# Kernel optimization log

Measured on AMD Instinct MI355X. Metric: run time of the kernel, lower is better.

## Reference

```python
import jax, jax.numpy as jnp
import numpy as np

N = 50000      # nodes
E = 800000     # edges (before self-loops)
H = 4          # heads
C = 64         # hidden_unit per head
IN = 256       # input_dim
OUT = 64       # output_dim
NEG = 0.2      # LeakyReLU slope in GATConv
EPS = 1e-5     # BatchNorm eps


def setup_inputs() -> dict:
    key = jax.random.key(0)
    ks = jax.random.split(key, 12)
    s = 0.05
    HC = H * C
    return {
        'x': jax.random.normal(ks[0], (N, IN), dtype=jnp.float32),
        'edge_index': jax.random.randint(ks[1], (2, E), 0, N, dtype=jnp.int64),
        # GATConv layer 1
        'W1': jax.random.normal(ks[2], (IN, HC), dtype=jnp.float32) * s,
        'att_src1': jax.random.normal(ks[3], (H, C), dtype=jnp.float32) * s,
        'att_dst1': jax.random.normal(ks[4], (H, C), dtype=jnp.float32) * s,
        'b1': jnp.zeros((HC,), jnp.float32),
        # GATConv layer 2
        'W2': jax.random.normal(ks[5], (HC, HC), dtype=jnp.float32) * s,
        'att_src2': jax.random.normal(ks[6], (H, C), dtype=jnp.float32) * s,
        'att_dst2': jax.random.normal(ks[7], (H, C), dtype=jnp.float32) * s,
        'b2': jnp.zeros((HC,), jnp.float32),
        # BatchNorms
        'g1': jnp.ones((HC,), jnp.float32), 'beta1': jnp.zeros((HC,), jnp.float32),
        'g2': jnp.ones((HC,), jnp.float32), 'beta2': jnp.zeros((HC,), jnp.float32),
        # final Linear
        'Wl': jax.random.normal(ks[8], (HC, OUT), dtype=jnp.float32) * s,
        'bl': jnp.zeros((OUT,), jnp.float32),
    }


def gat_layer(x, src, dst, W, a_src, a_dst, b):
    # x: [N, F_in] -> per-head features [N, H, C]
    xh = (x @ W).reshape(-1, H, C)
    alpha_src = jnp.einsum('nhc,hc->nh', xh, a_src)   # [N, H]
    alpha_dst = jnp.einsum('nhc,hc->nh', xh, a_dst)   # [N, H]
    e = jax.nn.leaky_relu(alpha_src[src] + alpha_dst[dst], NEG)  # [Etot, H]
    # segment softmax over edges grouped by destination node
    m = jax.ops.segment_max(e, dst, num_segments=N)              # [N, H]
    ex = jnp.exp(e - m[dst])
    den = jax.ops.segment_sum(ex, dst, num_segments=N)           # [N, H]
    alpha = ex / (den[dst] + 1e-16)                              # [Etot, H]
    # weighted scatter-add aggregation
    out = jax.ops.segment_sum(alpha[:, :, None] * xh[src], dst, num_segments=N)
    return out.reshape(-1, H * C) + b


def batchnorm(x, g, beta):
    mu = x.mean(axis=0)
    var = x.var(axis=0)
    return (x - mu) * jax.lax.rsqrt(var + EPS) * g + beta


def reference(x, edge_index, W1, att_src1, att_dst1, b1,
              W2, att_src2, att_dst2, b2, g1, beta1, g2, beta2, Wl, bl):
    # GATConv adds self-loops by default
    loops = jnp.arange(N, dtype=edge_index.dtype)
    src = jnp.concatenate([edge_index[0], loops])
    dst = jnp.concatenate([edge_index[1], loops])
    h = batchnorm(gat_layer(x, src, dst, W1, att_src1, att_dst1, b1), g1, beta1)
    # dropout is identity in eval mode
    h = batchnorm(gat_layer(h, src, dst, W2, att_src2, att_dst2, b2), g2, beta2)
    emb = h @ Wl + bl
    out = jax.nn.log_softmax(emb, axis=1)
    return (out, emb)
```

## Files before the change

### kernel.cpp

```cpp
#include <hip/hip_runtime.h>
#include <cstdint>

#define NNODES 50000
#define NEDGES 800000
#define ETOT   (NEDGES + NNODES)
#define HEADS 4
#define CH 64
#define HC 256
#define INDIM 256
#define OUTDIM 64
#define NEG_SLOPE 0.2f
#define BN_EPS 1e-5f
#define NB 128

typedef unsigned short u16;
typedef unsigned int u32;
typedef __attribute__((ext_vector_type(8))) short short8;
typedef __attribute__((ext_vector_type(8))) unsigned short ushort8v;
typedef __attribute__((ext_vector_type(4))) float floatx4;

__device__ inline float bf2f(u16 u) {
    union { unsigned int i; float f; } c;
    c.i = ((unsigned int)u) << 16;
    return c.f;
}
__device__ inline u16 f2bf(float f) {
    union { float f; unsigned int i; } c;
    c.f = f;
    unsigned int u = c.i + 0x7fff + ((c.i >> 16) & 1);
    return (u16)(u >> 16);
}
__device__ __host__ inline int pos256(int b) {
    int h = b >> 6, c = b & 63;
    return h * 64 + (c & 15) * 4 + (c >> 4);
}
__device__ inline void async16(u16* lds, const u16* g) {
    __builtin_amdgcn_global_load_lds(
        (const __attribute__((address_space(1))) unsigned int*)g,
        (__attribute__((address_space(3))) unsigned int*)lds,
        16, 0, 0);
}


__global__ void hist_kernel(const int* __restrict__ ei, int* __restrict__ cnt) {
    int t = blockIdx.x * blockDim.x + threadIdx.x;
    if (t >= ETOT) return;
    int d = (t < NEDGES) ? ei[NEDGES + t] : (t - NEDGES);
    atomicAdd(&cnt[d], 1);
}

__global__ void scan1_kernel(const int* __restrict__ cnt, int* __restrict__ row_off,
                             int* __restrict__ blockSums) {
    __shared__ int tsum[256];
    const int tid = threadIdx.x;
    const int base = blockIdx.x * 4096 + tid * 16;
    int local[16];
    int run = 0;
#pragma unroll
    for (int i = 0; i < 16; ++i) {
        int idx = base + i;
        int v = (idx < NNODES) ? cnt[idx] : 0;
        local[i] = run;
        run += v;
    }
    tsum[tid] = run;
    __syncthreads();
    for (int d = 1; d < 256; d <<= 1) {
        int v = (tid >= d) ? tsum[tid - d] : 0;
        __syncthreads();
        tsum[tid] += v;
        __syncthreads();
    }
    int excl = (tid == 0) ? 0 : tsum[tid - 1];
#pragma unroll
    for (int i = 0; i < 16; ++i) {
        int idx = base + i;
        if (idx < NNODES) row_off[idx] = excl + local[i];
    }
    if (tid == 0) blockSums[blockIdx.x] = tsum[255];
}

__global__ void scan2_kernel(int* __restrict__ row_off, const int* __restrict__ blockSums,
                             int* __restrict__ nxt) {
    __shared__ int sprefix;
    if (threadIdx.x == 0) {
        int p = 0;
        for (int b = 0; b < (int)blockIdx.x; ++b) p += blockSums[b];
        sprefix = p;
    }
    __syncthreads();
    int prefix = sprefix;
    int base = blockIdx.x * 4096 + threadIdx.x * 16;
#pragma unroll
    for (int i = 0; i < 16; ++i) {
        int idx = base + i;
        if (idx < NNODES) {
            int v = row_off[idx] + prefix;
            row_off[idx] = v;
            nxt[idx] = v;
        }
    }
    if (blockIdx.x == 0 && threadIdx.x == 0) row_off[NNODES] = ETOT;
}

#define FILL_S (ETOT / 4)
__global__ void fill_csr_kernel(const int* __restrict__ ei, int* __restrict__ nxt,
                                int* __restrict__ csr_src) {
    int t = blockIdx.x * blockDim.x + threadIdx.x;
    if (t >= FILL_S) return;
    int s[4], d[4], p[4];
#pragma unroll
    for (int k = 0; k < 4; ++k) {
        int e = t + k * FILL_S;
        if (e < NEDGES) { s[k] = ei[e]; d[k] = ei[NEDGES + e]; }
        else            { s[k] = d[k] = e - NEDGES; }
    }
#pragma unroll
    for (int k = 0; k < 4; ++k) p[k] = atomicAdd(&nxt[d[k]], 1);
#pragma unroll
    for (int k = 0; k < 4; ++k) csr_src[p[k]] = s[k];
}


__global__ void wcast_kernel(const float* __restrict__ W, u16* __restrict__ Wt,
                             int K, int Ncols) {
    int t = blockIdx.x * blockDim.x + threadIdx.x;
    if (t >= K * Ncols) return;
    int k = t / Ncols, n = t - k * Ncols;
    Wt[n * K + k] = f2bf(W[t]);
}


template <bool AF32>
__global__ __launch_bounds__(256)
void gemm_gat_kernel(const void* __restrict__ Ap, const u16* __restrict__ Bt,
                     const float* __restrict__ bias,
                     const float* __restrict__ att_s, const float* __restrict__ att_d,
                     u16* __restrict__ xhp, float* __restrict__ asrc,
                     float* __restrict__ adst, int M, int K) {
    __shared__ u16 As[128 * 32];
    __shared__ u16 Bs[128 * 32];
    const int tid = threadIdx.x;
    const int wave = tid >> 6, lane = tid & 63;
    const int q15 = lane & 15, quad = lane >> 4;
    const int rowBase = blockIdx.y * 128;
    const int colBase = blockIdx.x * 128;
    const int waveM = (wave >> 1) * 64, waveN = (wave & 1) * 64;
    const int head = blockIdx.x * 2 + (wave & 1);

    floatx4 acc[4][4];
    floatx4 zero = {0.f, 0.f, 0.f, 0.f};
#pragma unroll
    for (int i = 0; i < 4; ++i)
#pragma unroll
        for (int j = 0; j < 4; ++j) acc[i][j] = zero;

    for (int kt = 0; kt < K; kt += 32) {
        if constexpr (AF32) {
            const float* A32 = (const float*)Ap;
#pragma unroll
            for (int rnd = 0; rnd < 4; ++rnd) {
                int slot = rnd * 256 + tid;
                int r = slot >> 3, c4 = (slot & 7) * 4;
                int ar = rowBase + r; if (ar >= M) ar = M - 1;
                float4 fv = *(const float4*)&A32[(size_t)ar * K + kt + c4];
                ushort4 o;
                o.x = f2bf(fv.x); o.y = f2bf(fv.y); o.z = f2bf(fv.z); o.w = f2bf(fv.w);
                *(ushort4*)&As[r * 32 + c4] = o;
            }
#pragma unroll
            for (int q = 0; q < 2; ++q) {
                int e8 = (wave * 2 + q) * 64 + lane;
                int r = e8 >> 2, c = (e8 & 3) * 8;
                async16(&Bs[(wave * 2 + q) * 512], &Bt[(size_t)(colBase + r) * K + kt + c]);
            }
        } else {
            const u16* A16 = (const u16*)Ap;
#pragma unroll
            for (int q = 0; q < 2; ++q) {
                int e8 = (wave * 2 + q) * 64 + lane;
                int r = e8 >> 2, c = (e8 & 3) * 8;
                int ar = rowBase + r; if (ar >= M) ar = M - 1;
                async16(&As[(wave * 2 + q) * 512], &A16[(size_t)ar * K + kt + c]);
                async16(&Bs[(wave * 2 + q) * 512], &Bt[(size_t)(colBase + r) * K + kt + c]);
            }
        }
        __syncthreads();

        short8 af[4], bfr[4];
#pragma unroll
        for (int i = 0; i < 4; ++i)
            af[i] = *(const short8*)&As[(waveM + i * 16 + q15) * 32 + quad * 8];
#pragma unroll
        for (int j = 0; j < 4; ++j)
            bfr[j] = *(const short8*)&Bs[(waveN + j * 16 + q15) * 32 + quad * 8];
#pragma unroll
        for (int i = 0; i < 4; ++i)
#pragma unroll
            for (int j = 0; j < 4; ++j)
                acc[i][j] = __builtin_amdgcn_mfma_f32_16x16x32_bf16(af[i], bfr[j], acc[i][j], 0, 0, 0);
        __syncthreads();
    }

    float bv[4], atsv[4], atdv[4];
#pragma unroll
    for (int j = 0; j < 4; ++j) {
        int gcol = colBase + waveN + j * 16 + q15;
        bv[j] = bias ? bias[gcol] : 0.f;
        int hc = head * CH + j * 16 + q15;
        atsv[j] = att_s[hc];
        atdv[j] = att_d[hc];
    }
    const int pbase = head * 64 + q15 * 4;

#pragma unroll
    for (int i = 0; i < 4; ++i) {
#pragma unroll
        for (int rr = 0; rr < 4; ++rr) {
            int grow = rowBase + waveM + i * 16 + quad * 4 + rr;
            float v[4];
#pragma unroll
            for (int j = 0; j < 4; ++j) v[j] = acc[i][j][rr] + bv[j];
            float s = v[0] * atsv[0] + v[1] * atsv[1] + v[2] * atsv[2] + v[3] * atsv[3];
            float d = v[0] * atdv[0] + v[1] * atdv[1] + v[2] * atdv[2] + v[3] * atdv[3];
#pragma unroll
            for (int off = 1; off <= 8; off <<= 1) {
                s += __shfl_xor(s, off, 64);
                d += __shfl_xor(d, off, 64);
            }
            ushort4 o;
            o.x = f2bf(v[0]); o.y = f2bf(v[1]); o.z = f2bf(v[2]); o.w = f2bf(v[3]);
            if (grow < M) {
                *(ushort4*)&xhp[(size_t)grow * HC + pbase] = o;
                if (q15 == 0) {
                    asrc[grow * 4 + head] = s;
                    adst[grow * 4 + head] = d;
                }
            }
        }
    }
}


__global__ __launch_bounds__(256)
void aggregate_kernel(const int* __restrict__ row_off, const int* __restrict__ csr_src,
                      const float* __restrict__ asrc, const float* __restrict__ adst,
                      const u16* __restrict__ xhp, const float* __restrict__ bias,
                      u16* __restrict__ out) {
    const int g = threadIdx.x >> 6;
    const int lane = threadIdx.x & 63;
    const int d = blockIdx.x * 4 + g;
    const int h = lane >> 4;
    const int c16 = lane & 15;
    const int poff = h * 64 + c16 * 4;
    const int hsel = h & 2;
    const int hsh = (h & 1) * 16;
    const int start = row_off[d], end = row_off[d + 1];
    const float4 ad4 = *(const float4*)&adst[d * 4];
    float a0 = 0.f, a1 = 0.f, a2 = 0.f, a3 = 0.f, den = 0.f;

    for (int base = start; base < end; base += 64) {
        const int cnt = min(64, end - base);
        int sv = 0;
        u32 wx = 0, wy = 0;
        if (lane < cnt) {
            sv = csr_src[base + lane];
            float4 as4 = *(const float4*)&asrc[sv * 4];
            float e0 = as4.x + ad4.x; e0 = e0 > 0.f ? e0 : NEG_SLOPE * e0;
            float e1 = as4.y + ad4.y; e1 = e1 > 0.f ? e1 : NEG_SLOPE * e1;
            float e2 = as4.z + ad4.z; e2 = e2 > 0.f ? e2 : NEG_SLOPE * e2;
            float e3 = as4.w + ad4.w; e3 = e3 > 0.f ? e3 : NEG_SLOPE * e3;
            wx = (u32)f2bf(__expf(e0)) | ((u32)f2bf(__expf(e1)) << 16);
            wy = (u32)f2bf(__expf(e2)) | ((u32)f2bf(__expf(e3)) << 16);
        }
        int k = 0;
        for (; k + 3 < cnt; k += 4) {
            int s0 = __builtin_amdgcn_readlane(sv, k);
            int s1 = __builtin_amdgcn_readlane(sv, k + 1);
            int s2 = __builtin_amdgcn_readlane(sv, k + 2);
            int s3 = __builtin_amdgcn_readlane(sv, k + 3);
            u32 x0w = __builtin_amdgcn_readlane((int)wx, k), y0w = __builtin_amdgcn_readlane((int)wy, k);
            u32 x1w = __builtin_amdgcn_readlane((int)wx, k + 1), y1w = __builtin_amdgcn_readlane((int)wy, k + 1);
            u32 x2w = __builtin_amdgcn_readlane((int)wx, k + 2), y2w = __builtin_amdgcn_readlane((int)wy, k + 2);
            u32 x3w = __builtin_amdgcn_readlane((int)wx, k + 3), y3w = __builtin_amdgcn_readlane((int)wy, k + 3);
            ushort4 v0 = *(const ushort4*)&xhp[(size_t)s0 * HC + poff];
            ushort4 v1 = *(const ushort4*)&xhp[(size_t)s1 * HC + poff];
            ushort4 v2 = *(const ushort4*)&xhp[(size_t)s2 * HC + poff];
            ushort4 v3 = *(const ushort4*)&xhp[(size_t)s3 * HC + poff];
            float w0 = bf2f((u16)((hsel ? y0w : x0w) >> hsh));
            float w1 = bf2f((u16)((hsel ? y1w : x1w) >> hsh));
            float w2 = bf2f((u16)((hsel ? y2w : x2w) >> hsh));
            float w3 = bf2f((u16)((hsel ? y3w : x3w) >> hsh));
            den += (w0 + w1) + (w2 + w3);
            a0 += w0 * bf2f(v0.x) + w1 * bf2f(v1.x) + w2 * bf2f(v2.x) + w3 * bf2f(v3.x);
            a1 += w0 * bf2f(v0.y) + w1 * bf2f(v1.y) + w2 * bf2f(v2.y) + w3 * bf2f(v3.y);
            a2 += w0 * bf2f(v0.z) + w1 * bf2f(v1.z) + w2 * bf2f(v2.z) + w3 * bf2f(v3.z);
            a3 += w0 * bf2f(v0.w) + w1 * bf2f(v1.w) + w2 * bf2f(v2.w) + w3 * bf2f(v3.w);
        }
        for (; k < cnt; ++k) {
            int s0 = __builtin_amdgcn_readlane(sv, k);
            u32 x0w = __builtin_amdgcn_readlane((int)wx, k), y0w = __builtin_amdgcn_readlane((int)wy, k);
            ushort4 v0 = *(const ushort4*)&xhp[(size_t)s0 * HC + poff];
            float w0 = bf2f((u16)((hsel ? y0w : x0w) >> hsh));
            den += w0;
            a0 += w0 * bf2f(v0.x);
            a1 += w0 * bf2f(v0.y);
            a2 += w0 * bf2f(v0.z);
            a3 += w0 * bf2f(v0.w);
        }
    }
    float inv = 1.f / (den + 1e-16f);
    const int ch0 = h * 64 + c16;
    ushort4 o;
    o.x = f2bf(a0 * inv + bias[ch0 +  0]);
    o.y = f2bf(a1 * inv + bias[ch0 + 16]);
    o.z = f2bf(a2 * inv + bias[ch0 + 32]);
    o.w = f2bf(a3 * inv + bias[ch0 + 48]);
    *(ushort4*)&out[(size_t)d * HC + poff] = o;
}


__global__ __launch_bounds__(256)
void bn_stats_kernel(const u16* __restrict__ x, float* __restrict__ part) {
    const int tid = threadIdx.x;
    float s[8] = {}, s2[8] = {};
    const size_t total = (size_t)NNODES * HC;
    const size_t stride = (size_t)NB * 256 * 8;
    for (size_t f = ((size_t)blockIdx.x * 256 + tid) * 8; f < total; f += stride) {
        ushort8v v = *(const ushort8v*)&x[f];
#pragma unroll
        for (int i = 0; i < 8; ++i) {
            float t = bf2f(v[i]);
            s[i] += t;
            s2[i] += t * t;
        }
    }
#pragma unroll
    for (int i = 0; i < 8; ++i) {
        s[i] += __shfl_xor(s[i], 32, 64);
        s2[i] += __shfl_xor(s2[i], 32, 64);
    }
    __shared__ float red[4][512];
    const int wave = tid >> 6, lane = tid & 63;
    if (lane < 32) {
#pragma unroll
        for (int i = 0; i < 8; ++i) {
            red[wave][lane * 8 + i] = s[i];
            red[wave][256 + lane * 8 + i] = s2[i];
        }
    }
    __syncthreads();
    for (int j = tid; j < 512; j += 256)
        part[(size_t)blockIdx.x * 512 + j] = red[0][j] + red[1][j] + red[2][j] + red[3][j];
}


__global__ __launch_bounds__(256)
void fold_kernel(const float* __restrict__ W, const float* __restrict__ part,
                 const float* __restrict__ g, const float* __restrict__ beta,
                 const float* __restrict__ baseBias,
                 u16* __restrict__ Wt, float* __restrict__ biasOut, int Ncols) {
    __shared__ float sh[256];
    __shared__ float stat2[2];
    const int b = blockIdx.x;
    const int tid = threadIdx.x;
    if (b < 256) {
        const int p = pos256(b);
        const int wave = tid >> 6, lane = tid & 63;
        if (wave < 2) {
            int off = wave * 256;
            float v = part[(size_t)lane * 512 + off + p] + part[(size_t)(lane + 64) * 512 + off + p];
#pragma unroll
            for (int o = 1; o <= 32; o <<= 1) v += __shfl_xor(v, o, 64);
            if (lane == 0) stat2[wave] = v;
        }
        __syncthreads();
        float mu = stat2[0] * (1.f / NNODES);
        float var = stat2[1] * (1.f / NNODES) - mu * mu;
        float rg = rsqrtf(var + BN_EPS) * g[b];
        for (int n = tid; n < Ncols; n += 256)
            Wt[n * 256 + p] = f2bf(W[b * Ncols + n] * rg);
    } else {
        const int p = pos256(tid);
        float sum = 0.f, sq = 0.f;
        for (int k = 0; k < NB; ++k) {
            sum += part[(size_t)k * 512 + p];
            sq += part[(size_t)k * 512 + 256 + p];
        }
        float mu = sum * (1.f / NNODES);
        float var = sq * (1.f / NNODES) - mu * mu;
        float rg = rsqrtf(var + BN_EPS) * g[tid];
        sh[tid] = beta[tid] - mu * rg;
        __syncthreads();
        if (tid < Ncols) {
            float acc = baseBias ? baseBias[tid] : 0.f;
            for (int k = 0; k < 256; ++k) acc += sh[k] * W[k * Ncols + tid];
            biasOut[tid] = acc;
        }
    }
}


__global__ __launch_bounds__(256)
void final_ls_kernel(const u16* __restrict__ A, const u16* __restrict__ Bt,
                     const float* __restrict__ bias,
                     float* __restrict__ emb, float* __restrict__ out, int M) {
    __shared__ u16 As[128 * 32];
    __shared__ u16 Bs[64 * 32];
    const int tid = threadIdx.x;
    const int wave = tid >> 6, lane = tid & 63;
    const int q15 = lane & 15, quad = lane >> 4;
    const int rowBase = blockIdx.x * 128;

    floatx4 acc[2][4];
    floatx4 zero = {0.f, 0.f, 0.f, 0.f};
#pragma unroll
    for (int i = 0; i < 2; ++i)
#pragma unroll
        for (int j = 0; j < 4; ++j) acc[i][j] = zero;

    for (int kt = 0; kt < 256; kt += 32) {
#pragma unroll
        for (int rnd = 0; rnd < 2; ++rnd) {
            int slot = rnd * 256 + wave * 64 + lane;
            int r = slot >> 2;
            int c = (slot & 3) * 8;
            int ar = rowBase + r; if (ar >= M) ar = M - 1;
            async16(&As[(rnd * 256 + wave * 64) * 8], &A[(size_t)ar * 256 + kt + c]);
        }
        {
            int slot = wave * 64 + lane;
            int r = slot >> 2;
            int c = (slot & 3) * 8;
            async16(&Bs[(wave * 64) * 8], &Bt[(size_t)r * 256 + kt + c]);
        }
        __syncthreads();

        short8 af[2], bfr[4];
#pragma unroll
        for (int i = 0; i < 2; ++i)
            af[i] = *(const short8*)&As[(wave * 32 + i * 16 + q15) * 32 + quad * 8];
#pragma unroll
        for (int j = 0; j < 4; ++j)
            bfr[j] = *(const short8*)&Bs[(j * 16 + q15) * 32 + quad * 8];
#pragma unroll
        for (int i = 0; i < 2; ++i)
#pragma unroll
            for (int j = 0; j < 4; ++j)
                acc[i][j] = __builtin_amdgcn_mfma_f32_16x16x32_bf16(af[i], bfr[j], acc[i][j], 0, 0, 0);
        __syncthreads();
    }

#pragma unroll
    for (int i = 0; i < 2; ++i) {
#pragma unroll
        for (int rr = 0; rr < 4; ++rr) {
            float v[4];
#pragma unroll
            for (int j = 0; j < 4; ++j) v[j] = acc[i][j][rr] + bias[j * 16 + q15];
            float m = fmaxf(fmaxf(v[0], v[1]), fmaxf(v[2], v[3]));
#pragma unroll
            for (int off = 1; off <= 8; off <<= 1) m = fmaxf(m, __shfl_xor(m, off, 64));
            float s = __expf(v[0] - m) + __expf(v[1] - m) + __expf(v[2] - m) + __expf(v[3] - m);
#pragma unroll
            for (int off = 1; off <= 8; off <<= 1) s += __shfl_xor(s, off, 64);
            float ls = m + logf(s);
            int grow = rowBase + wave * 32 + i * 16 + quad * 4 + rr;
            if (grow < M) {
#pragma unroll
                for (int j = 0; j < 4; ++j) {
                    int col = j * 16 + q15;
                    emb[(size_t)grow * OUTDIM + col] = v[j];
                    out[(size_t)grow * OUTDIM + col] = v[j] - ls;
                }
            }
        }
    }
}


extern "C" void kernel_launch(void* const* d_in, const int* in_sizes, int n_in,
                              void* d_out, int out_size, void* d_ws, size_t ws_size,
                              hipStream_t stream) {
    const float* x   = (const float*)d_in[0];
    const int*   ei  = (const int*)d_in[1];
    const float* W1  = (const float*)d_in[2];
    const float* at_s1 = (const float*)d_in[3];
    const float* at_d1 = (const float*)d_in[4];
    const float* b1  = (const float*)d_in[5];
    const float* W2  = (const float*)d_in[6];
    const float* at_s2 = (const float*)d_in[7];
    const float* at_d2 = (const float*)d_in[8];
    const float* b2  = (const float*)d_in[9];
    const float* g1  = (const float*)d_in[10];
    const float* be1 = (const float*)d_in[11];
    const float* g2  = (const float*)d_in[12];
    const float* be2 = (const float*)d_in[13];
    const float* Wl  = (const float*)d_in[14];
    const float* bl  = (const float*)d_in[15];

    float* out = (float*)d_out;
    float* emb = out + (size_t)NNODES * OUTDIM;

    char* ws = (char*)d_ws;
    size_t off = 0;
    auto alloc = [&](size_t bytes) {
        void* p = ws + off;
        off += (bytes + 255) & ~(size_t)255;
        return p;
    };
    int*   cnt     = (int*)alloc((size_t)NNODES * 4);
    int*   row_off = (int*)alloc((size_t)(NNODES + 1) * 4);
    int*   nxt     = (int*)alloc((size_t)NNODES * 4);
    int*   bsums   = (int*)alloc(64 * 4);
    int*   csr_src = (int*)alloc((size_t)ETOT * 4);
    float* asrc    = (float*)alloc((size_t)NNODES * 4 * 4);
    float* adst    = (float*)alloc((size_t)NNODES * 4 * 4);
    u16*   xhp     = (u16*)alloc((size_t)NNODES * HC * 2);
    u16*   ag_bf   = (u16*)alloc((size_t)NNODES * HC * 2);
    u16*   w1t     = (u16*)alloc((size_t)HC * INDIM * 2);
    u16*   w2t     = (u16*)alloc((size_t)HC * HC * 2);
    u16*   wlt     = (u16*)alloc((size_t)OUTDIM * HC * 2);
    float* part    = (float*)alloc((size_t)NB * 512 * 4);
    float* bias2   = (float*)alloc(HC * 4);
    float* blp     = (float*)alloc(OUTDIM * 4);

    const int scanBlocks = (NNODES + 4095) / 4096;
    const int eBlocks = (ETOT + 255) / 256;

    hipMemsetAsync(cnt, 0, (size_t)NNODES * 4, stream);
    hist_kernel<<<eBlocks, 256, 0, stream>>>(ei, cnt);
    scan1_kernel<<<scanBlocks, 256, 0, stream>>>(cnt, row_off, bsums);
    scan2_kernel<<<scanBlocks, 256, 0, stream>>>(row_off, bsums, nxt);
    fill_csr_kernel<<<(FILL_S + 255) / 256, 256, 0, stream>>>(ei, nxt, csr_src);

    wcast_kernel<<<(INDIM * HC + 255) / 256, 256, 0, stream>>>(W1, w1t, INDIM, HC);

    dim3 gemmGrid(2, (NNODES + 127) / 128);

    gemm_gat_kernel<true><<<gemmGrid, 256, 0, stream>>>(x, w1t, nullptr, at_s1, at_d1,
                                                        xhp, asrc, adst, NNODES, INDIM);
    aggregate_kernel<<<NNODES / 4, 256, 0, stream>>>(row_off, csr_src, asrc, adst, xhp, b1, ag_bf);
    bn_stats_kernel<<<NB, 256, 0, stream>>>(ag_bf, part);
    fold_kernel<<<257, 256, 0, stream>>>(W2, part, g1, be1, nullptr, w2t, bias2, HC);

    gemm_gat_kernel<false><<<gemmGrid, 256, 0, stream>>>(ag_bf, w2t, bias2, at_s2, at_d2,
                                                         xhp, asrc, adst, NNODES, HC);
    aggregate_kernel<<<NNODES / 4, 256, 0, stream>>>(row_off, csr_src, asrc, adst, xhp, b2, ag_bf);
    bn_stats_kernel<<<NB, 256, 0, stream>>>(ag_bf, part);
    fold_kernel<<<257, 256, 0, stream>>>(Wl, part, g2, be2, bl, wlt, blp, OUTDIM);

    final_ls_kernel<<<(NNODES + 127) / 128, 256, 0, stream>>>(ag_bf, wlt, blp, emb, out, NNODES);
}
```

Baseline: 500.2 us.

## Split aggregation wave into two half-waves with 16-byte gathers and LDS-staged weights

Result: no change. 495.0 us (-1.0%).

```diff
diff --git a/kernel.cpp b/kernel.cpp
--- a/kernel.cpp
+++ b/kernel.cpp
@@ -247,76 +247,97 @@
                       const float* __restrict__ asrc, const float* __restrict__ adst,
                       const u16* __restrict__ xhp, const float* __restrict__ bias,
                       u16* __restrict__ out) {
+    __shared__ int eb[4][512];
     const int g = threadIdx.x >> 6;
     const int lane = threadIdx.x & 63;
     const int d = blockIdx.x * 4 + g;
-    const int h = lane >> 4;
-    const int c16 = lane & 15;
-    const int poff = h * 64 + c16 * 4;
-    const int hsel = h & 2;
-    const int hsh = (h & 1) * 16;
+    const int eh = lane >> 5;
+    const int L = lane & 31;
+    const int h = L >> 3;
+    const int g8 = L & 7;
+    const u32 pb = (u32)(h * 128 + g8 * 16);
+    int* my = &eb[g][0];
+
     const int start = row_off[d], end = row_off[d + 1];
     const float4 ad4 = *(const float4*)&adst[d * 4];
-    float a0 = 0.f, a1 = 0.f, a2 = 0.f, a3 = 0.f, den = 0.f;
+    float acc[8] = {0.f, 0.f, 0.f, 0.f, 0.f, 0.f, 0.f, 0.f};
+    float den = 0.f;
+
+#define ACC4(W, Q, J0) { u32 dw_ = (u32)(Q); \
+        acc[J0]     += (W) * __int_as_float(dw_ << 16); \
+        acc[(J0)+1] += (W) * __int_as_float(dw_ & 0xffff0000u); }
 
     for (int base = start; base < end; base += 64) {
         const int cnt = min(64, end - base);
-        int sv = 0;
-        u32 wx = 0, wy = 0;
+        int4 pack = {0, 0, 0, 0};
+        int svv = 0;
         if (lane < cnt) {
-            sv = csr_src[base + lane];
-            float4 as4 = *(const float4*)&asrc[sv * 4];
+            svv = csr_src[base + lane];
+            float4 as4 = *(const float4*)&asrc[svv * 4];
             float e0 = as4.x + ad4.x; e0 = e0 > 0.f ? e0 : NEG_SLOPE * e0;
             float e1 = as4.y + ad4.y; e1 = e1 > 0.f ? e1 : NEG_SLOPE * e1;
             float e2 = as4.z + ad4.z; e2 = e2 > 0.f ? e2 : NEG_SLOPE * e2;
             float e3 = as4.w + ad4.w; e3 = e3 > 0.f ? e3 : NEG_SLOPE * e3;
-            wx = (u32)f2bf(__expf(e0)) | ((u32)f2bf(__expf(e1)) << 16);
-            wy = (u32)f2bf(__expf(e2)) | ((u32)f2bf(__expf(e3)) << 16);
-        }
+            pack.x = __float_as_int(__expf(e0));
+            pack.y = __float_as_int(__expf(e1));
+            pack.z = __float_as_int(__expf(e2));
+            pack.w = __float_as_int(__expf(e3));
+        }
+        *(int4*)&my[lane * 8] = pack;
+        my[lane * 8 + 4] = svv;
+        asm volatile("s_waitcnt lgkmcnt(0)" ::: "memory");
+        __builtin_amdgcn_sched_barrier(0);
+
+        const int cntp = (cnt + 1) & ~1;
         int k = 0;
-        for (; k + 3 < cnt; k += 4) {
-            int s0 = __builtin_amdgcn_readlane(sv, k);
-            int s1 = __builtin_amdgcn_readlane(sv, k + 1);
-            int s2 = __builtin_amdgcn_readlane(sv, k + 2);
-            int s3 = __builtin_amdgcn_readlane(sv, k + 3);
-            u32 x0w = __builtin_amdgcn_readlane((int)wx, k), y0w = __builtin_amdgcn_readlane((int)wy, k);
-            u32 x1w = __builtin_amdgcn_readlane((int)wx, k + 1), y1w = __builtin_amdgcn_readlane((int)wy, k + 1);
-            u32 x2w = __builtin_amdgcn_readlane((int)wx, k + 2), y2w = __builtin_amdgcn_readlane((int)wy, k + 2);
-            u32 x3w = __builtin_amdgcn_readlane((int)wx, k + 3), y3w = __builtin_amdgcn_readlane((int)wy, k + 3);
-            ushort4 v0 = *(const ushort4*)&xhp[(size_t)s0 * HC + poff];
-            ushort4 v1 = *(const ushort4*)&xhp[(size_t)s1 * HC + poff];
-            ushort4 v2 = *(const ushort4*)&xhp[(size_t)s2 * HC + poff];
-            ushort4 v3 = *(const ushort4*)&xhp[(size_t)s3 * HC + poff];
-            float w0 = bf2f((u16)((hsel ? y0w : x0w) >> hsh));
-            float w1 = bf2f((u16)((hsel ? y1w : x1w) >> hsh));
-            float w2 = bf2f((u16)((hsel ? y2w : x2w) >> hsh));
-            float w3 = bf2f((u16)((hsel ? y3w : x3w) >> hsh));
-            den += (w0 + w1) + (w2 + w3);
-            a0 += w0 * bf2f(v0.x) + w1 * bf2f(v1.x) + w2 * bf2f(v2.x) + w3 * bf2f(v3.x);
-            a1 += w0 * bf2f(v0.y) + w1 * bf2f(v1.y) + w2 * bf2f(v2.y) + w3 * bf2f(v3.y);
-            a2 += w0 * bf2f(v0.z) + w1 * bf2f(v1.z) + w2 * bf2f(v2.z) + w3 * bf2f(v3.z);
-            a3 += w0 * bf2f(v0.w) + w1 * bf2f(v1.w) + w2 * bf2f(v2.w) + w3 * bf2f(v3.w);
-        }
-        for (; k < cnt; ++k) {
-            int s0 = __builtin_amdgcn_readlane(sv, k);
-            u32 x0w = __builtin_amdgcn_readlane((int)wx, k), y0w = __builtin_amdgcn_readlane((int)wy, k);
-            ushort4 v0 = *(const ushort4*)&xhp[(size_t)s0 * HC + poff];
-            float w0 = bf2f((u16)((hsel ? y0w : x0w) >> hsh));
-            den += w0;
-            a0 += w0 * bf2f(v0.x);
-            a1 += w0 * bf2f(v0.y);
-            a2 += w0 * bf2f(v0.z);
-            a3 += w0 * bf2f(v0.w);
-        }
-    }
-    float inv = 1.f / (den + 1e-16f);
-    const int ch0 = h * 64 + c16;
-    ushort4 o;
-    o.x = f2bf(a0 * inv + bias[ch0 +  0]);
-    o.y = f2bf(a1 * inv + bias[ch0 + 16]);
-    o.z = f2bf(a2 * inv + bias[ch0 + 32]);
-    o.w = f2bf(a3 * inv + bias[ch0 + 48]);
-    *(ushort4*)&out[(size_t)d * HC + poff] = o;
+        for (; k + 7 < cntp; k += 8) {
+            float wv[4]; int sa[4];
+#pragma unroll
+            for (int p = 0; p < 4; ++p) {
+                int idx = (k + 2 * p + eh) * 8;
+                wv[p] = __int_as_float(my[idx + h]);
+                sa[p] = my[idx + 4];
+            }
+            int4 gv[4];
+#pragma unroll
+            for (int p = 0; p < 4; ++p) {
+                u32 off = ((u32)sa[p] << 9) + pb;
+                gv[p] = *(const int4*)((const char*)xhp + off);
+            }
+#pragma unroll
+            for (int p = 0; p < 4; ++p) {
+                float w = wv[p];
+                den += w;
+                ACC4(w, gv[p].x, 0); ACC4(w, gv[p].y, 2);
+                ACC4(w, gv[p].z, 4); ACC4(w, gv[p].w, 6);
+            }
+        }
+        for (; k < cntp; k += 2) {
+            int idx = (k + eh) * 8;
+            float w = __int_as_float(my[idx + h]);
+            int s = my[idx + 4];
+            u32 off = ((u32)s << 9) + pb;
+            int4 gvv = *(const int4*)((const char*)xhp + off);
+            den += w;
+            ACC4(w, gvv.x, 0); ACC4(w, gvv.y, 2);
+            ACC4(w, gvv.z, 4); ACC4(w, gvv.w, 6);
+        }
+    }
+#undef ACC4
+
+#pragma unroll
+    for (int i = 0; i < 8; ++i) acc[i] += __shfl_xor(acc[i], 32, 64);
+    den += __shfl_xor(den, 32, 64);
+
+    if (eh == 0) {
+        float inv = 1.f / (den + 1e-16f);
+        const int cb = h * 64 + g8 * 2;
+        ushort8v o;
+#pragma unroll
+        for (int j = 0; j < 8; ++j)
+            o[j] = f2bf(acc[j] * inv + bias[cb + (j >> 2) + (j & 3) * 16]);
+        *(ushort8v*)&out[(size_t)d * HC + h * 64 + g8 * 8] = o;
+    }
 }
 
 
```
